# Kernel tuning notes

Hardware: AMD Instinct MI355X
Metric: run time of the kernel (lower is better)

## Reference

```python
import jax, jax.numpy as jnp
import numpy as np
import math

B, NTR, NTE = 4, 256, 64
S = NTR + NTE
FN, D = 64, 256
HF, HS = 8, 8
HC = HF // 2
HID = 4 * D


def _ln(x, g, b, eps=1e-5):
    m = jnp.mean(x, axis=-1, keepdims=True)
    v = jnp.mean((x - m) ** 2, axis=-1, keepdims=True)
    return (x - m) / jnp.sqrt(v + eps) * g + b


def _mha(q, k, v, Wq, bq, Wk, bk, Wv, bv, Wo, bo, H, mask):
    # PyTorch nn.MultiheadAttention (batch_first, eval): per-head scaled dot product
    Bq, Lq, Dm = q.shape
    Lk = k.shape[1]
    hd = Dm // H
    qh = (q @ Wq.T + bq).reshape(Bq, Lq, H, hd).transpose(0, 2, 1, 3)
    kh = (k @ Wk.T + bk).reshape(Bq, Lk, H, hd).transpose(0, 2, 1, 3)
    vh = (v @ Wv.T + bv).reshape(Bq, Lk, H, hd).transpose(0, 2, 1, 3)
    s = jnp.einsum('bhqd,bhkd->bhqk', qh, kh) / math.sqrt(hd)
    if mask is not None:
        s = s + mask  # broadcast (1,H,Lq,Lk)
    a = jax.nn.softmax(s, axis=-1)
    o = jnp.einsum('bhqk,bhkd->bhqd', a, vh).transpose(0, 2, 1, 3).reshape(Bq, Lq, Dm)
    return o @ Wo.T + bo


def setup_inputs() -> dict:
    key = jax.random.key(0)
    ks = jax.random.split(key, 64)
    i = [0]
    def w(shape, s=0.02):
        k = ks[i[0]]; i[0] += 1
        return jax.random.normal(k, shape, jnp.float32) * s
    inp = {}
    inp['x'] = jax.random.normal(ks[40], (B, S, FN, D), jnp.float32)
    m = jax.random.randint(ks[41], (FN, FN), 0, 2).astype(jnp.float32)
    inp['attn_mask'] = jnp.maximum(m, jnp.eye(FN, dtype=jnp.float32))  # keep diagonal unmasked
    for p in ['f', 't', 'e']:
        for n in ['Wq', 'Wk', 'Wv', 'Wo']:
            inp[n + p] = w((D, D))
        for n in ['bq', 'bk', 'bv', 'bo']:
            inp[n + p] = jnp.zeros((D,), jnp.float32)
        inp['g' + p] = jnp.ones((D,), jnp.float32)
        inp['b2' + p] = jnp.zeros((D,), jnp.float32)
    inp['W1'] = w((HID, D)); inp['b1'] = jnp.zeros((HID,), jnp.float32)
    inp['Wg'] = w((HID, D)); inp['bg'] = jnp.zeros((HID,), jnp.float32)
    inp['W2'] = w((D, HID)); inp['b2'] = jnp.zeros((D,), jnp.float32)
    inp['gm'] = jnp.ones((D,), jnp.float32); inp['bm'] = jnp.zeros((D,), jnp.float32)
    inp['N_train'] = NTR
    inp['N_test'] = NTE
    return inp


def reference(x, attn_mask, Wqf, Wkf, Wvf, Wof, bqf, bkf, bvf, bof, gf, b2f,
              Wqt, Wkt, Wvt, Wot, bqt, bkt, bvt, bot, gt, b2t,
              Wqe, Wke, Wve, Woe, bqe, bke, bve, boe, ge, b2e,
              W1, b1, Wg, bg, W2, b2, gm, bm, N_train, N_test):
    Bsz, Ssz, Fn, Dd = x.shape
    # --- feature attention with hybrid per-head mask ---
    x_row = x.reshape(Bsz * Ssz, Fn, Dd)
    xn = _ln(x_row, gf, b2f)
    additive = jnp.where(attn_mask == 1.0, 0.0, -jnp.inf).astype(x.dtype)  # (F,F)
    hybrid = jnp.concatenate([
        jnp.broadcast_to(additive[None], (HC, Fn, Fn)),
        jnp.zeros((HF - HC, Fn, Fn), x.dtype)], axis=0)[None]  # (1,H,F,F)
    x2 = _mha(xn, xn, xn, Wqf, bqf, Wkf, bkf, Wvf, bvf, Wof, bof, HF, hybrid)
    x_row = x_row + x2
    # --- sample attention (train self, test cross) ---
    x_col = x_row.reshape(Bsz, Ssz, Fn, Dd).transpose(0, 2, 1, 3).reshape(Bsz * Fn, Ssz, Dd)
    x_tr = x_col[:, :N_train]
    x_te = x_col[:, N_train:]
    tn = _ln(x_tr, gt, b2t)
    x_tr = x_tr + _mha(tn, tn, tn, Wqt, bqt, Wkt, bkt, Wvt, bvt, Wot, bot, HS, None)
    en = _ln(x_te, ge, b2e)
    kv = _ln(x_tr, ge, b2e)
    x_te = x_te + _mha(en, kv, kv, Wqe, bqe, Wke, bke, Wve, bve, Woe, boe, HS, None)
    x_col = jnp.concatenate([x_tr, x_te], axis=1)
    xo = x_col.reshape(Bsz, Fn, Ssz, Dd).transpose(0, 2, 1, 3)
    # --- SwiGLU MLP ---
    xn2 = _ln(xo, gm, bm)
    h = (xn2 @ W1.T + b1) * jax.nn.silu(xn2 @ Wg.T + bg)
    return xo + (h @ W2.T + b2)
```

## Files before the change

kernel.cpp:

```cpp
#include <hip/hip_runtime.h>
#include <hip/hip_bf16.h>

typedef __hip_bfloat16 bf16;
typedef __attribute__((ext_vector_type(8))) short short8v;
typedef __attribute__((ext_vector_type(4))) float f32x4;

#define Bz   4
#define Sz   320
#define FNz  64
#define Dz   256
#define HIDz 1024
#define TOK  (Bz*Sz*FNz)
#define NSEQ (Bz*FNz)
#define NTRz 256
#define NTEz 64
#define TTR  (NSEQ*NTRz)
#define TTE  (NSEQ*NTEz)
#define CHD  40960
#define SCALE 0.17677669529663687f

__device__ __forceinline__ size_t rowOff(int rr, int Ls, int s0){
  if (Ls == 0) return (size_t)rr * Dz;
  int n = rr / Ls;
  int s = rr - n * Ls + s0;
  return (((size_t)(n >> 6) * Sz + s) * FNz + (n & 63)) * Dz;
}

__device__ __forceinline__ void store4bf(bf16* p, float a, float b, float c, float d){
  bf16 t0=__float2bfloat16(a), t1=__float2bfloat16(b),
       t2=__float2bfloat16(c), t3=__float2bfloat16(d);
  ushort4 u;
  u.x=*(unsigned short*)&t0; u.y=*(unsigned short*)&t1;
  u.z=*(unsigned short*)&t2; u.w=*(unsigned short*)&t3;
  *(ushort4*)p = u;
}

__device__ __forceinline__ void store2bf(bf16* p, float a, float b){
  bf16 t0=__float2bfloat16(a), t1=__float2bfloat16(b);
  ushort2 u;
  u.x=*(unsigned short*)&t0; u.y=*(unsigned short*)&t1;
  *(ushort2*)p = u;
}

__device__ __forceinline__ void xcd_work(int ncols, int& row, int& col){
  int L   = blockIdx.x;
  int cpx = gridDim.x >> 3;
  int W   = (L & 7) * cpx + (L >> 3);
  row = W / ncols;
  col = W - row * ncols;
}

struct CvtArgs { const float* src[24]; bf16* dst[24]; };
__global__ __launch_bounds__(256) void cvt_multi(CvtArgs args){
  int i = (blockIdx.x * 256 + threadIdx.x) * 4;
  const float* s = args.src[blockIdx.y];
  bf16*        d = args.dst[blockIdx.y];
  float4 v = *(const float4*)(s + i);
  store4bf(d + i, v.x, v.y, v.z, v.w);
}

__global__ __launch_bounds__(256) void ln_kernel(const float* __restrict__ src,
    bf16* __restrict__ dst, const float* __restrict__ g, const float* __restrict__ b,
    int Ls, int s0){
  int rr   = blockIdx.x * 4 + (threadIdx.x >> 6);
  int lane = threadIdx.x & 63;
  size_t off = rowOff(rr, Ls, s0) + (size_t)lane * 4;
  float4 v = *(const float4*)(src + off);
  float s = v.x + v.y + v.z + v.w;
  float q = v.x*v.x + v.y*v.y + v.z*v.z + v.w*v.w;
  #pragma unroll
  for (int d = 1; d < 64; d <<= 1){ s += __shfl_xor(s, d); q += __shfl_xor(q, d); }
  float m   = s * (1.0f/Dz);
  float rsd = rsqrtf(q * (1.0f/Dz) - m*m + 1e-5f);
  float4 gv = *(const float4*)(g + lane*4);
  float4 bv = *(const float4*)(b + lane*4);
  store4bf(dst + (size_t)rr*Dz + lane*4,
           (v.x-m)*rsd*gv.x + bv.x, (v.y-m)*rsd*gv.y + bv.y,
           (v.z-m)*rsd*gv.z + bv.z, (v.w-m)*rsd*gv.w + bv.w);
}

template<int EPI>
__global__ __launch_bounds__(512) void mgemm(
    const bf16* __restrict__ A, const bf16* __restrict__ Wb,
    const float* __restrict__ bias, const float* __restrict__ biasB,
    const float* __restrict__ biasC, void* __restrict__ Cp,
    const float* __restrict__ resid, const bf16* __restrict__ aux,
    int M, int N, int K, int cLs, int cS0, int ncols){
  __shared__ __align__(16) char smemraw[30720];
  bf16 (*As)[40] = reinterpret_cast<bf16(*)[40]>(smemraw);
  bf16 (*Bs)[40] = reinterpret_cast<bf16(*)[40]>(smemraw + 10240);
  const int tid  = threadIdx.x;
  const int lane = tid & 63;
  const int wave = tid >> 6;
  int rowb, colb;
  xcd_work(ncols, rowb, colb);
  const int r0 = rowb * 128;
  const int n0 = colb * 256;
  const int srow = tid >> 2;
  const int scol = (tid & 3) * 8;
  const int bprow = (srow & 64) + (srow & 15)*4 + ((srow >> 4) & 3);
  const bf16* ap  = A  + (size_t)(r0 + srow) * K + scol;
  const bf16* bp0 = Wb + (size_t)(n0 + bprow) * K + scol;
  const bf16* bp1 = Wb + (size_t)(n0 + 128 + bprow) * K + scol;
  const int wr = wave >> 2, wc = wave & 3;
  const int fr = lane & 15;
  const int fk = (lane >> 4) * 8;
  f32x4 acc[4][4] = {};
  for (int k0 = 0; k0 < K; k0 += 32){
    uint4 av  = *(const uint4*)(ap  + k0);
    uint4 bv0 = *(const uint4*)(bp0 + k0);
    uint4 bv1 = *(const uint4*)(bp1 + k0);
    __syncthreads();
    *(uint4*)&As[srow][scol]       = av;
    *(uint4*)&Bs[srow][scol]       = bv0;
    *(uint4*)&Bs[128 + srow][scol] = bv1;
    __syncthreads();
    short8v af[4], bf[4];
    #pragma unroll
    for (int m = 0; m < 4; ++m)
      af[m] = *(const short8v*)&As[wr*64 + m*16 + fr][fk];
    #pragma unroll
    for (int n = 0; n < 4; ++n)
      bf[n] = *(const short8v*)&Bs[wc*64 + n*16 + fr][fk];
    #pragma unroll
    for (int m = 0; m < 4; ++m)
      #pragma unroll
      for (int n = 0; n < 4; ++n)
        acc[m][n] = __builtin_amdgcn_mfma_f32_16x16x32_bf16(af[m], bf[n], acc[m][n], 0, 0, 0);
  }
  const int er = (lane >> 4) * 4;
  if (EPI == 1){
    float* fsm = (float*)smemraw;
    const int cb = wc*64 + fr*4;
    float bb0 = bias[cb], bb1 = bias[cb+1], bb2 = bias[cb+2], bb3 = bias[cb+3];
    #pragma unroll
    for (int m = 0; m < 4; ++m){
      #pragma unroll
      for (int wrs = 0; wrs < 2; ++wrs){
        __syncthreads();
        if (wr == wrs){
          #pragma unroll
          for (int j = 0; j < 4; ++j){
            float4 t;
            t.x = acc[m][0][j] + bb0; t.y = acc[m][1][j] + bb1;
            t.z = acc[m][2][j] + bb2; t.w = acc[m][3][j] + bb3;
            *(float4*)&fsm[(er + j)*260 + cb] = t;
          }
        }
        __syncthreads();
        int rrow = r0 + wrs*64 + m*16 + (tid >> 5);
        size_t ro = rowOff(rrow, cLs, cS0) + (size_t)(tid & 31)*8;
        const float* fs = fsm + (tid >> 5)*260 + (tid & 31)*8;
        float4 v0 = *(const float4*)(fs);
        float4 v1 = *(const float4*)(fs + 4);
        float4 q0 = *(const float4*)(resid + ro);
        float4 q1 = *(const float4*)(resid + ro + 4);
        v0.x += q0.x; v0.y += q0.y; v0.z += q0.z; v0.w += q0.w;
        v1.x += q1.x; v1.y += q1.y; v1.z += q1.z; v1.w += q1.w;
        *(float4*)((float*)Cp + ro)     = v0;
        *(float4*)((float*)Cp + ro + 4) = v1;
      }
    }
  } else {
    const float* bp = bias;
    if (biasB != nullptr) bp = (colb == 0) ? bias : ((colb == 1) ? biasB : biasC);
    const int cl = wc*64 + fr*4;
    float bb0 = bp[cl], bb1 = bp[cl+1], bb2 = bp[cl+2], bb3 = bp[cl+3];
    const int cbase = n0 + cl;
    #pragma unroll
    for (int m = 0; m < 4; ++m){
      #pragma unroll
      for (int j = 0; j < 4; ++j){
        int r = r0 + wr*64 + m*16 + er + j;
        store4bf(&((bf16*)Cp)[(size_t)r * N + cbase],
                 acc[m][0][j] + bb0, acc[m][1][j] + bb1,
                 acc[m][2][j] + bb2, acc[m][3][j] + bb3);
      }
    }
  }
}

__global__ __launch_bounds__(512) void mgemm_dual(
    const bf16* __restrict__ A, const bf16* __restrict__ W1b,
    const bf16* __restrict__ Wgb, const float* __restrict__ b1,
    const float* __restrict__ bg, bf16* __restrict__ Hb,
    int M, int K){
  __shared__ bf16 As[128][40];
  __shared__ bf16 B1s[128][40];
  __shared__ bf16 B2s[128][40];
  const int tid  = threadIdx.x;
  const int lane = tid & 63;
  const int wave = tid >> 6;
  int rowb, colb;
  xcd_work(8, rowb, colb);
  const int r0 = rowb * 128;
  const int n0 = colb * 128;
  const int srow = tid >> 2;
  const int scol = (tid & 3) * 8;
  const int bprow = (srow & ~31) + (srow & 15)*2 + ((srow >> 4) & 1);
  const bf16* ap = A   + (size_t)(r0 + srow) * K + scol;
  const bf16* p1 = W1b + (size_t)(n0 + bprow) * K + scol;
  const bf16* p2 = Wgb + (size_t)(n0 + bprow) * K + scol;
  const int wr = wave >> 2, wc = wave & 3;
  const int fr = lane & 15;
  const int fk = (lane >> 4) * 8;
  f32x4 acc1[4][2] = {};
  f32x4 acc2[4][2] = {};
  for (int k0 = 0; k0 < K; k0 += 32){
    uint4 av = *(const uint4*)(ap + k0);
    uint4 v1 = *(const uint4*)(p1 + k0);
    uint4 v2 = *(const uint4*)(p2 + k0);
    __syncthreads();
    *(uint4*)&As[srow][scol]  = av;
    *(uint4*)&B1s[srow][scol] = v1;
    *(uint4*)&B2s[srow][scol] = v2;
    __syncthreads();
    short8v af[4], bf1[2], bf2[2];
    #pragma unroll
    for (int m = 0; m < 4; ++m)
      af[m] = *(const short8v*)&As[wr*64 + m*16 + fr][fk];
    #pragma unroll
    for (int n = 0; n < 2; ++n){
      bf1[n] = *(const short8v*)&B1s[wc*32 + n*16 + fr][fk];
      bf2[n] = *(const short8v*)&B2s[wc*32 + n*16 + fr][fk];
    }
    #pragma unroll
    for (int m = 0; m < 4; ++m)
      #pragma unroll
      for (int n = 0; n < 2; ++n){
        acc1[m][n] = __builtin_amdgcn_mfma_f32_16x16x32_bf16(af[m], bf1[n], acc1[m][n], 0, 0, 0);
        acc2[m][n] = __builtin_amdgcn_mfma_f32_16x16x32_bf16(af[m], bf2[n], acc2[m][n], 0, 0, 0);
      }
  }
  const int er = (lane >> 4) * 4;
  const int c = n0 + wc*32 + fr*2;
  const float b10 = b1[c], b11 = b1[c+1];
  const float bg0 = bg[c], bg1 = bg[c+1];
  #pragma unroll
  for (int m = 0; m < 4; ++m){
    #pragma unroll
    for (int j = 0; j < 4; ++j){
      int r = r0 + wr*64 + m*16 + er + j;
      float v0 = acc1[m][0][j] + b10;
      float g0 = acc2[m][0][j] + bg0;
      float v1 = acc1[m][1][j] + b11;
      float g1 = acc2[m][1][j] + bg1;
      float h0 = v0 * g0 / (1.0f + __expf(-g0));
      float h1 = v1 * g1 / (1.0f + __expf(-g1));
      store2bf(&Hb[(size_t)r * HIDz + c], h0, h1);
    }
  }
}

__global__ __launch_bounds__(256) void attn_t_m(
    const bf16* __restrict__ Q, const bf16* __restrict__ K,
    const bf16* __restrict__ V, bf16* __restrict__ O, int ld){
  __shared__ bf16 Klds[64][40];
  __shared__ bf16 Vt[32][72];
  __shared__ bf16 Plds[4][64][72];
  const int n = blockIdx.x, h = blockIdx.y;
  const int tid = threadIdx.x, lane = tid & 63, w = tid >> 6;
  const size_t ibase = (size_t)n * 256 * ld + (size_t)h * 32;
  const size_t obase = (size_t)n * 256 * Dz + (size_t)h * 32;
  const int l15 = lane & 15, l4 = lane >> 4;
  short8v qf[4];
  #pragma unroll
  for (int m = 0; m < 4; ++m)
    qf[m] = *(const short8v*)(Q + ibase + (size_t)(w*64 + m*16 + l15) * ld + l4*8);
  f32x4 accO[4][2] = {};
  float mrowq[4], lrowq[4], sclq[4];
  #pragma unroll
  for (int m=0;m<4;++m){ mrowq[m] = -1e30f; lrowq[m] = 0.f; }
  const f32x4 zero = {};
  for (int kb = 0; kb < 4; ++kb){
    __syncthreads();
    {
      int r = tid >> 2, c8 = (tid & 3) * 8;
      *(uint4*)&Klds[r][c8] = *(const uint4*)(K + ibase + (size_t)(kb*64 + r) * ld + c8);
      uint4 vr = *(const uint4*)(V + ibase + (size_t)(kb*64 + r) * ld + c8);
      const bf16* vb = (const bf16*)&vr;
      #pragma unroll
      for (int i = 0; i < 8; ++i) Vt[c8 + i][r] = vb[i];
    }
    __syncthreads();
    short8v kf[4];
    #pragma unroll
    for (int nn = 0; nn < 4; ++nn)
      kf[nn] = *(const short8v*)&Klds[nn*16 + l15][l4*8];
    f32x4 s2[4][4];
    #pragma unroll
    for (int m = 0; m < 4; ++m)
      #pragma unroll
      for (int nn = 0; nn < 4; ++nn)
        s2[m][nn] = __builtin_amdgcn_mfma_f32_16x16x32_bf16(kf[nn], qf[m], zero, 0,0,0);
    #pragma unroll
    for (int m = 0; m < 4; ++m){
      float mx = fmaxf(fmaxf(s2[m][0][0], s2[m][0][1]), fmaxf(s2[m][0][2], s2[m][0][3]));
      #pragma unroll
      for (int nn = 1; nn < 4; ++nn)
        mx = fmaxf(mx, fmaxf(fmaxf(s2[m][nn][0], s2[m][nn][1]),
                             fmaxf(s2[m][nn][2], s2[m][nn][3])));
      mx = fmaxf(mx, __shfl_xor(mx, 16));
      mx = fmaxf(mx, __shfl_xor(mx, 32));
      float mnew = fmaxf(mrowq[m], mx);
      float scl = __expf((mrowq[m] - mnew) * SCALE);
      mrowq[m] = mnew; sclq[m] = scl;
      float ps = 0.f;
      #pragma unroll
      for (int nn = 0; nn < 4; ++nn)
        #pragma unroll
        for (int j = 0; j < 4; ++j){
          float p = __expf((s2[m][nn][j] - mnew) * SCALE);
          s2[m][nn][j] = p; ps += p;
        }
      ps += __shfl_xor(ps, 16);
      ps += __shfl_xor(ps, 32);
      lrowq[m] = lrowq[m] * scl + ps;
    }
    #pragma unroll
    for (int m = 0; m < 4; ++m)
      #pragma unroll
      for (int j = 0; j < 4; ++j){
        float so = __shfl(sclq[m], l4*4 + j);
        accO[m][0][j] *= so; accO[m][1][j] *= so;
      }
    #pragma unroll
    for (int m = 0; m < 4; ++m)
      #pragma unroll
      for (int nn = 0; nn < 4; ++nn)
        store4bf(&Plds[w][m*16 + l15][nn*16 + l4*4],
                 s2[m][nn][0], s2[m][nn][1], s2[m][nn][2], s2[m][nn][3]);
    #pragma unroll
    for (int m = 0; m < 4; ++m){
      #pragma unroll
      for (int kt = 0; kt < 2; ++kt){
        short8v pf = *(const short8v*)&Plds[w][m*16 + l15][kt*32 + l4*8];
        #pragma unroll
        for (int dt = 0; dt < 2; ++dt){
          short8v vf = *(const short8v*)&Vt[dt*16 + l15][kt*32 + l4*8];
          accO[m][dt] = __builtin_amdgcn_mfma_f32_16x16x32_bf16(pf, vf, accO[m][dt], 0,0,0);
        }
      }
    }
  }
  #pragma unroll
  for (int m = 0; m < 4; ++m){
    #pragma unroll
    for (int j = 0; j < 4; ++j){
      float inv = 1.0f / __shfl(lrowq[m], l4*4 + j);
      int row = w*64 + m*16 + l4*4 + j;
      #pragma unroll
      for (int dt = 0; dt < 2; ++dt)
        O[obase + (size_t)row * Dz + dt*16 + l15] = __float2bfloat16(accO[m][dt][j] * inv);
    }
  }
}

template<int NKB, int MASK>
__global__ __launch_bounds__(256) void attn_w(
    const bf16* __restrict__ Q, const bf16* __restrict__ K,
    const bf16* __restrict__ V, const float* __restrict__ mask,
    bf16* __restrict__ O, int ldq, int ldkv){
  __shared__ bf16 Klds[4][64][40];
  __shared__ bf16 Vt[4][32][72];
  __shared__ bf16 Plds[4][64][72];
  const int r = blockIdx.x;
  const int tid = threadIdx.x, lane = tid & 63, w = tid >> 6;
  const int h = blockIdx.y * 4 + w;
  const int l15 = lane & 15, l4 = lane >> 4;
  const size_t qoff = (size_t)r * 64 * ldq + (size_t)h * 32;
  const size_t koff = (size_t)r * (NKB*64) * ldkv + (size_t)h * 32;
  const size_t ooff = (size_t)r * 64 * Dz + (size_t)h * 32;
  short8v qf[4];
  #pragma unroll
  for (int m = 0; m < 4; ++m)
    qf[m] = *(const short8v*)(Q + qoff + (size_t)(m*16 + l15) * ldq + l4*8);
  f32x4 accO[4][2] = {};
  float mrowq[4], lrowq[4], sclq[4];
  #pragma unroll
  for (int m=0;m<4;++m){ mrowq[m] = -1e30f; lrowq[m] = 0.f; }
  const f32x4 zero = {};
  for (int kb = 0; kb < NKB; ++kb){
    {
      const bf16* kp = K + koff + (size_t)(kb*64 + lane) * ldkv;
      const bf16* vp = V + koff + (size_t)(kb*64 + lane) * ldkv;
      uint4 k0 = *(const uint4*)(kp);      uint4 k1 = *(const uint4*)(kp + 8);
      uint4 k2 = *(const uint4*)(kp + 16); uint4 k3 = *(const uint4*)(kp + 24);
      *(uint4*)&Klds[w][lane][0]  = k0; *(uint4*)&Klds[w][lane][8]  = k1;
      *(uint4*)&Klds[w][lane][16] = k2; *(uint4*)&Klds[w][lane][24] = k3;
      uint4 v0 = *(const uint4*)(vp);      uint4 v1 = *(const uint4*)(vp + 8);
      uint4 v2 = *(const uint4*)(vp + 16); uint4 v3 = *(const uint4*)(vp + 24);
      const bf16* vb0=(const bf16*)&v0; const bf16* vb1=(const bf16*)&v1;
      const bf16* vb2=(const bf16*)&v2; const bf16* vb3=(const bf16*)&v3;
      #pragma unroll
      for (int i = 0; i < 8; ++i){
        Vt[w][i][lane]      = vb0[i];
        Vt[w][8 + i][lane]  = vb1[i];
        Vt[w][16 + i][lane] = vb2[i];
        Vt[w][24 + i][lane] = vb3[i];
      }
    }
    short8v kf[4];
    #pragma unroll
    for (int nn = 0; nn < 4; ++nn)
      kf[nn] = *(const short8v*)&Klds[w][nn*16 + l15][l4*8];
    f32x4 s2[4][4];
    #pragma unroll
    for (int m = 0; m < 4; ++m)
      #pragma unroll
      for (int nn = 0; nn < 4; ++nn)
        s2[m][nn] = __builtin_amdgcn_mfma_f32_16x16x32_bf16(kf[nn], qf[m], zero, 0,0,0);
    if (MASK && h < 4){
      #pragma unroll
      for (int m = 0; m < 4; ++m)
        #pragma unroll
        for (int nn = 0; nn < 4; ++nn)
          #pragma unroll
          for (int j = 0; j < 4; ++j){
            int qq = m*16 + l15, kk = nn*16 + l4*4 + j;
            s2[m][nn][j] += (mask[qq*64 + kk] == 1.0f ? 0.0f : -1e30f);
          }
    }
    #pragma unroll
    for (int m = 0; m < 4; ++m){
      float mx = fmaxf(fmaxf(s2[m][0][0], s2[m][0][1]), fmaxf(s2[m][0][2], s2[m][0][3]));
      #pragma unroll
      for (int nn = 1; nn < 4; ++nn)
        mx = fmaxf(mx, fmaxf(fmaxf(s2[m][nn][0], s2[m][nn][1]),
                             fmaxf(s2[m][nn][2], s2[m][nn][3])));
      mx = fmaxf(mx, __shfl_xor(mx, 16));
      mx = fmaxf(mx, __shfl_xor(mx, 32));
      float mnew = fmaxf(mrowq[m], mx);
      float scl = __expf((mrowq[m] - mnew) * SCALE);
      mrowq[m] = mnew; sclq[m] = scl;
      float ps = 0.f;
      #pragma unroll
      for (int nn = 0; nn < 4; ++nn)
        #pragma unroll
        for (int j = 0; j < 4; ++j){
          float p = __expf((s2[m][nn][j] - mnew) * SCALE);
          s2[m][nn][j] = p; ps += p;
        }
      ps += __shfl_xor(ps, 16);
      ps += __shfl_xor(ps, 32);
      lrowq[m] = lrowq[m] * scl + ps;
    }
    #pragma unroll
    for (int m = 0; m < 4; ++m)
      #pragma unroll
      for (int j = 0; j < 4; ++j){
        float so = __shfl(sclq[m], l4*4 + j);
        accO[m][0][j] *= so; accO[m][1][j] *= so;
      }
    #pragma unroll
    for (int m = 0; m < 4; ++m)
      #pragma unroll
      for (int nn = 0; nn < 4; ++nn)
        store4bf(&Plds[w][m*16 + l15][nn*16 + l4*4],
                 s2[m][nn][0], s2[m][nn][1], s2[m][nn][2], s2[m][nn][3]);
    #pragma unroll
    for (int m = 0; m < 4; ++m){
      #pragma unroll
      for (int kt = 0; kt < 2; ++kt){
        short8v pf = *(const short8v*)&Plds[w][m*16 + l15][kt*32 + l4*8];
        #pragma unroll
        for (int dt = 0; dt < 2; ++dt){
          short8v vf = *(const short8v*)&Vt[w][dt*16 + l15][kt*32 + l4*8];
          accO[m][dt] = __builtin_amdgcn_mfma_f32_16x16x32_bf16(pf, vf, accO[m][dt], 0,0,0);
        }
      }
    }
  }
  #pragma unroll
  for (int m = 0; m < 4; ++m){
    #pragma unroll
    for (int j = 0; j < 4; ++j){
      float inv = 1.0f / __shfl(lrowq[m], l4*4 + j);
      int row = m*16 + l4*4 + j;
      #pragma unroll
      for (int dt = 0; dt < 2; ++dt)
        O[ooff + (size_t)row * Dz + dt*16 + l15] = __float2bfloat16(accO[m][dt][j] * inv);
    }
  }
}

extern "C" void kernel_launch(void* const* d_in, const int* in_sizes, int n_in,
                              void* d_out, int out_size, void* d_ws, size_t ws_size,
                              hipStream_t stream){
  (void)in_sizes; (void)n_in; (void)out_size; (void)ws_size;
  const float* x    = (const float*)d_in[0];
  const float* mask = (const float*)d_in[1];
  const float *Wqf=(const float*)d_in[2],  *Wkf=(const float*)d_in[3],
              *Wvf=(const float*)d_in[4],  *Wof=(const float*)d_in[5],
              *bqf=(const float*)d_in[6],  *bkf=(const float*)d_in[7],
              *bvf=(const float*)d_in[8],  *bof=(const float*)d_in[9],
              *gf =(const float*)d_in[10], *b2f=(const float*)d_in[11];
  const float *Wqt=(const float*)d_in[12], *Wkt=(const float*)d_in[13],
              *Wvt=(const float*)d_in[14], *Wot=(const float*)d_in[15],
              *bqt=(const float*)d_in[16], *bkt=(const float*)d_in[17],
              *bvt=(const float*)d_in[18], *bot=(const float*)d_in[19],
              *gt =(const float*)d_in[20], *b2t=(const float*)d_in[21];
  const float *Wqe=(const float*)d_in[22], *Wke=(const float*)d_in[23],
              *Wve=(const float*)d_in[24], *Woe=(const float*)d_in[25],
              *bqe=(const float*)d_in[26], *bke=(const float*)d_in[27],
              *bve=(const float*)d_in[28], *boe=(const float*)d_in[29],
              *ge =(const float*)d_in[30], *b2e=(const float*)d_in[31];
  const float *W1=(const float*)d_in[32], *b1=(const float*)d_in[33],
              *Wg=(const float*)d_in[34], *bg=(const float*)d_in[35],
              *W2=(const float*)d_in[36], *b2v=(const float*)d_in[37],
              *gm=(const float*)d_in[38], *bm=(const float*)d_in[39];

  float* Y = (float*)d_out;

  char* wsb = (char*)d_ws;
  size_t off = 0;
  auto carve = [&](size_t bytes)->void*{
    void* p = wsb + off; off += (bytes + 255) & ~(size_t)255; return p;
  };
  bf16* Xn   = (bf16*)carve((size_t)TOK * Dz * 2);
  bf16* QKVb = (bf16*)carve((size_t)TOK * 768 * 2);
  bf16* Ob   = (bf16*)carve((size_t)TOK * Dz * 2);
  bf16* Hb   = (bf16*)carve((size_t)CHD * HIDz * 2);
  bf16* WQKVf = (bf16*)carve((size_t)768*256*2);
  bf16* WQKVt = (bf16*)carve((size_t)768*256*2);
  bf16* WKVe  = (bf16*)carve((size_t)512*256*2);
  bf16* Wqeb  = (bf16*)carve((size_t)256*256*2);
  bf16* Wofb  = (bf16*)carve((size_t)256*256*2);
  bf16* Wotb  = (bf16*)carve((size_t)256*256*2);
  bf16* Woeb  = (bf16*)carve((size_t)256*256*2);
  bf16* W1b   = (bf16*)carve((size_t)HIDz*256*2);
  bf16* Wgb   = (bf16*)carve((size_t)HIDz*256*2);
  bf16* W2b   = (bf16*)carve((size_t)256*HIDz*2);

  const int DD = Dz*Dz;
  {
    CvtArgs ca;
    const float* s12[12] = {Wqf,Wkf,Wvf, Wqt,Wkt,Wvt, Wke,Wve, Wqe,Wof,Wot,Woe};
    bf16* d12[12] = {WQKVf,WQKVf+DD,WQKVf+2*DD, WQKVt,WQKVt+DD,WQKVt+2*DD,
                     WKVe,WKVe+DD, Wqeb,Wofb,Wotb,Woeb};
    for (int i = 0; i < 12; ++i){ ca.src[i] = s12[i]; ca.dst[i] = d12[i]; }
    const float* sh[3] = {W1, Wg, W2};
    bf16* dh[3] = {W1b, Wgb, W2b};
    for (int j = 0; j < 3; ++j)
      for (int p = 0; p < 4; ++p){
        ca.src[12 + j*4 + p] = sh[j] + (size_t)p * DD;
        ca.dst[12 + j*4 + p] = dh[j] + (size_t)p * DD;
      }
    cvt_multi<<<dim3(DD/1024, 24), 256, 0, stream>>>(ca);
  }

  bf16* Qeb = QKVb + (size_t)TTR * 512;

  ln_kernel<<<TOK/4, 256, 0, stream>>>(x, Xn, gf, b2f, 0, 0);
  mgemm<0><<<3*(TOK/128), 512, 0, stream>>>(Xn, WQKVf, bqf, bkf, bvf, QKVb,
      nullptr, nullptr, TOK, 768, 256, 0,0, 3);
  attn_w<1,1><<<dim3(Bz*Sz, 2), 256, 0, stream>>>(QKVb, QKVb+256, QKVb+512, mask, Ob, 768, 768);
  mgemm<1><<<TOK/128, 512, 0, stream>>>(Ob, Wofb, bof, nullptr, nullptr, Y,
      x, nullptr, TOK, 256, 256, 0,0, 1);

  ln_kernel<<<TTR/4, 256, 0, stream>>>(Y, Xn, gt, b2t, NTRz, 0);
  mgemm<0><<<3*(TTR/128), 512, 0, stream>>>(Xn, WQKVt, bqt, bkt, bvt, QKVb,
      nullptr, nullptr, TTR, 768, 256, 0,0, 3);
  attn_t_m<<<dim3(NSEQ, 8), 256, 0, stream>>>(QKVb, QKVb+256, QKVb+512, Ob, 768);
  mgemm<1><<<TTR/128, 512, 0, stream>>>(Ob, Wotb, bot, nullptr, nullptr, Y,
      Y, nullptr, TTR, 256, 256, NTRz,0, 1);

  ln_kernel<<<TTR/4, 256, 0, stream>>>(Y, Xn, ge, b2e, NTRz, 0);
  ln_kernel<<<TTE/4, 256, 0, stream>>>(Y, Xn + (size_t)TTR*Dz, ge, b2e, NTEz, NTRz);
  mgemm<0><<<TTE/128, 512, 0, stream>>>(Xn + (size_t)TTR*Dz, Wqeb, bqe,
      nullptr, nullptr, Qeb, nullptr, nullptr, TTE, 256, 256, 0,0, 1);
  mgemm<0><<<2*(TTR/128), 512, 0, stream>>>(Xn, WKVe, bke, bve, bve, QKVb,
      nullptr, nullptr, TTR, 512, 256, 0,0, 2);
  attn_w<4,0><<<dim3(NSEQ, 2), 256, 0, stream>>>(Qeb, QKVb, QKVb+256, nullptr, Ob, 256, 512);
  mgemm<1><<<TTE/128, 512, 0, stream>>>(Ob, Woeb, boe, nullptr, nullptr, Y,
      Y, nullptr, TTE, 256, 256, NTEz,NTRz, 1);

  ln_kernel<<<TOK/4, 256, 0, stream>>>(Y, Xn, gm, bm, 0, 0);
  for (int c = 0; c < TOK/CHD; ++c){
    const bf16* Anc = Xn + (size_t)c * CHD * Dz;
    float*      Yc  = Y  + (size_t)c * CHD * Dz;
    mgemm_dual<<<8*(CHD/128), 512, 0, stream>>>(Anc, W1b, Wgb, b1, bg,
        Hb, CHD, 256);
    mgemm<1><<<CHD/128, 512, 0, stream>>>(Hb, W2b, b2v, nullptr, nullptr,
        Yc, Yc, nullptr, CHD, 256, HIDz, 0,0, 1);
  }
}
```

Measured before the change: 719.9 us.

## Fuse downstream LayerNorms into residual-add GEMM epilogues

```diff
diff --git a/kernel.cpp b/kernel.cpp
--- a/kernel.cpp
+++ b/kernel.cpp
@@ -50,6 +50,28 @@
   col = W - row * ncols;
 }
 
+__device__ __forceinline__ void halfwave_ln(float4 v0, float4 v1,
+                                            float& mean, float& rsd){
+  float s = v0.x+v0.y+v0.z+v0.w + v1.x+v1.y+v1.z+v1.w;
+  float q = v0.x*v0.x+v0.y*v0.y+v0.z*v0.z+v0.w*v0.w
+          + v1.x*v1.x+v1.y*v1.y+v1.z*v1.z+v1.w*v1.w;
+  #pragma unroll
+  for (int d = 1; d < 32; d <<= 1){ s += __shfl_xor(s, d); q += __shfl_xor(q, d); }
+  mean = s * (1.0f/Dz);
+  rsd  = rsqrtf(q * (1.0f/Dz) - mean*mean + 1e-5f);
+}
+
+__device__ __forceinline__ void ln_emit(bf16* dp, int c0, float4 v0, float4 v1,
+                                        float mean, float rsd,
+                                        const float* G, const float* B){
+  float4 g0 = *(const float4*)(G + c0), g1 = *(const float4*)(G + c0 + 4);
+  float4 b0 = *(const float4*)(B + c0), b1 = *(const float4*)(B + c0 + 4);
+  store4bf(dp + c0,     (v0.x-mean)*rsd*g0.x + b0.x, (v0.y-mean)*rsd*g0.y + b0.y,
+                        (v0.z-mean)*rsd*g0.z + b0.z, (v0.w-mean)*rsd*g0.w + b0.w);
+  store4bf(dp + c0 + 4, (v1.x-mean)*rsd*g1.x + b1.x, (v1.y-mean)*rsd*g1.y + b1.y,
+                        (v1.z-mean)*rsd*g1.z + b1.z, (v1.w-mean)*rsd*g1.w + b1.w);
+}
+
 struct CvtArgs { const float* src[24]; bf16* dst[24]; };
 __global__ __launch_bounds__(256) void cvt_multi(CvtArgs args){
   int i = (blockIdx.x * 256 + threadIdx.x) * 4;
@@ -79,13 +101,15 @@
            (v.z-m)*rsd*gv.z + bv.z, (v.w-m)*rsd*gv.w + bv.w);
 }
 
-template<int EPI>
+template<int EPI, int FUSE>
 __global__ __launch_bounds__(512) void mgemm(
     const bf16* __restrict__ A, const bf16* __restrict__ Wb,
     const float* __restrict__ bias, const float* __restrict__ biasB,
     const float* __restrict__ biasC, void* __restrict__ Cp,
     const float* __restrict__ resid, const bf16* __restrict__ aux,
-    int M, int N, int K, int cLs, int cS0, int ncols){
+    int M, int N, int K, int cLs, int cS0, int ncols,
+    const float* lnGa, const float* lnBa, const float* lnGb, const float* lnBb,
+    bf16* dstA, bf16* dstB){
   __shared__ __align__(16) char smemraw[30720];
   bf16 (*As)[40] = reinterpret_cast<bf16(*)[40]>(smemraw);
   bf16 (*Bs)[40] = reinterpret_cast<bf16(*)[40]>(smemraw + 10240);
@@ -149,8 +173,9 @@
         }
         __syncthreads();
         int rrow = r0 + wrs*64 + m*16 + (tid >> 5);
-        size_t ro = rowOff(rrow, cLs, cS0) + (size_t)(tid & 31)*8;
-        const float* fs = fsm + (tid >> 5)*260 + (tid & 31)*8;
+        int c0 = (tid & 31) * 8;
+        size_t ro = rowOff(rrow, cLs, cS0) + c0;
+        const float* fs = fsm + (tid >> 5)*260 + c0;
         float4 v0 = *(const float4*)(fs);
         float4 v1 = *(const float4*)(fs + 4);
         float4 q0 = *(const float4*)(resid + ro);
@@ -159,6 +184,29 @@
         v1.x += q1.x; v1.y += q1.y; v1.z += q1.z; v1.w += q1.w;
         *(float4*)((float*)Cp + ro)     = v0;
         *(float4*)((float*)Cp + ro + 4) = v1;
+        if (FUSE > 0){
+          float mean, rsd;
+          halfwave_ln(v0, v1, mean, rsd);
+          if (FUSE == 1){
+            int b = rrow / (Sz*FNz);
+            int rem = rrow - b*(Sz*FNz);
+            int s = rem >> 6, f = rem & 63;
+            int n = (b << 6) + f;
+            if (s < NTRz)
+              ln_emit(dstA + (size_t)(n*NTRz + s)*Dz, c0, v0, v1, mean, rsd, lnGa, lnBa);
+            else
+              ln_emit(dstB + (size_t)(n*NTEz + s - NTRz)*Dz, c0, v0, v1, mean, rsd, lnGb, lnBb);
+          } else if (FUSE == 2){
+            int n = rrow >> 8, s = rrow & 255;
+            int b = n >> 6, f = n & 63;
+            ln_emit(dstA + (size_t)rrow*Dz, c0, v0, v1, mean, rsd, lnGa, lnBa);
+            ln_emit(dstB + (size_t)((b*Sz + s)*FNz + f)*Dz, c0, v0, v1, mean, rsd, lnGb, lnBb);
+          } else {
+            int n = rrow >> 6, t = rrow & 63;
+            int b = n >> 6, f = n & 63, s = t + NTRz;
+            ln_emit(dstB + (size_t)((b*Sz + s)*FNz + f)*Dz, c0, v0, v1, mean, rsd, lnGb, lnBb);
+          }
+        }
       }
     }
   } else {
@@ -532,6 +580,10 @@
   bf16* Wgb   = (bf16*)carve((size_t)HIDz*256*2);
   bf16* W2b   = (bf16*)carve((size_t)256*HIDz*2);
 
+  bf16* XnD = QKVb + (size_t)TOK * 512;
+  bf16* Xnq = Xn + (size_t)TTR * Dz;
+  bf16* Qeb = QKVb + (size_t)TTR * 512;
+
   const int DD = Dz*Dz;
   {
     CvtArgs ca;
@@ -549,39 +601,42 @@
     cvt_multi<<<dim3(DD/1024, 24), 256, 0, stream>>>(ca);
   }
 
-  bf16* Qeb = QKVb + (size_t)TTR * 512;
-
   ln_kernel<<<TOK/4, 256, 0, stream>>>(x, Xn, gf, b2f, 0, 0);
-  mgemm<0><<<3*(TOK/128), 512, 0, stream>>>(Xn, WQKVf, bqf, bkf, bvf, QKVb,
-      nullptr, nullptr, TOK, 768, 256, 0,0, 3);
+  mgemm<0,0><<<3*(TOK/128), 512, 0, stream>>>(Xn, WQKVf, bqf, bkf, bvf, QKVb,
+      nullptr, nullptr, TOK, 768, 256, 0,0, 3,
+      nullptr,nullptr,nullptr,nullptr, nullptr,nullptr);
   attn_w<1,1><<<dim3(Bz*Sz, 2), 256, 0, stream>>>(QKVb, QKVb+256, QKVb+512, mask, Ob, 768, 768);
-  mgemm<1><<<TOK/128, 512, 0, stream>>>(Ob, Wofb, bof, nullptr, nullptr, Y,
-      x, nullptr, TOK, 256, 256, 0,0, 1);
-
-  ln_kernel<<<TTR/4, 256, 0, stream>>>(Y, Xn, gt, b2t, NTRz, 0);
-  mgemm<0><<<3*(TTR/128), 512, 0, stream>>>(Xn, WQKVt, bqt, bkt, bvt, QKVb,
-      nullptr, nullptr, TTR, 768, 256, 0,0, 3);
+  mgemm<1,1><<<TOK/128, 512, 0, stream>>>(Ob, Wofb, bof, nullptr, nullptr, Y,
+      x, nullptr, TOK, 256, 256, 0,0, 1,
+      gt, b2t, ge, b2e, Xn, Xnq);
+
+  mgemm<0,0><<<3*(TTR/128), 512, 0, stream>>>(Xn, WQKVt, bqt, bkt, bvt, QKVb,
+      nullptr, nullptr, TTR, 768, 256, 0,0, 3,
+      nullptr,nullptr,nullptr,nullptr, nullptr,nullptr);
   attn_t_m<<<dim3(NSEQ, 8), 256, 0, stream>>>(QKVb, QKVb+256, QKVb+512, Ob, 768);
-  mgemm<1><<<TTR/128, 512, 0, stream>>>(Ob, Wotb, bot, nullptr, nullptr, Y,
-      Y, nullptr, TTR, 256, 256, NTRz,0, 1);
-
-  ln_kernel<<<TTR/4, 256, 0, stream>>>(Y, Xn, ge, b2e, NTRz, 0);
-  ln_kernel<<<TTE/4, 256, 0, stream>>>(Y, Xn + (size_t)TTR*Dz, ge, b2e, NTEz, NTRz);
-  mgemm<0><<<TTE/128, 512, 0, stream>>>(Xn + (size_t)TTR*Dz, Wqeb, bqe,
-      nullptr, nullptr, Qeb, nullptr, nullptr, TTE, 256, 256, 0,0, 1);
-  mgemm<0><<<2*(TTR/128), 512, 0, stream>>>(Xn, WKVe, bke, bve, bve, QKVb,
-      nullptr, nullptr, TTR, 512, 256, 0,0, 2);
-  attn_w<4,0><<<dim3(NSEQ, 2), 256, 0, stream>>>(Qeb, QKVb, QKVb+256, nullptr, Ob, 256, 512);
-  mgemm<1><<<TTE/128, 512, 0, stream>>>(Ob, Woeb, boe, nullptr, nullptr, Y,
-      Y, nullptr, TTE, 256, 256, NTEz,NTRz, 1);
-
-  ln_kernel<<<TOK/4, 256, 0, stream>>>(Y, Xn, gm, bm, 0, 0);
+  mgemm<1,2><<<TTR/128, 512, 0, stream>>>(Ob, Wotb, bot, nullptr, nullptr, Y,
+      Y, nullptr, TTR, 256, 256, NTRz,0, 1,
+      ge, b2e, gm, bm, Xn, XnD);
+
+  mgemm<0,0><<<TTE/128, 512, 0, stream>>>(Xnq, Wqeb, bqe,
+      nullptr, nullptr, Qeb, nullptr, nullptr, TTE, 256, 256, 0,0, 1,
+      nullptr,nullptr,nullptr,nullptr, nullptr,nullptr);
+  mgemm<0,0><<<2*(TTR/128), 512, 0, stream>>>(Xn, WKVe, bke, bve, bve, QKVb,
+      nullptr, nullptr, TTR, 512, 256, 0,0, 2,
+      nullptr,nullptr,nullptr,nullptr, nullptr,nullptr);
+  attn_w<4,0><<<dim3(NSEQ, 2), 256, 0, stream>>>(Qeb, QKVb, QKVb+256,
+      nullptr, Ob, 256, 512);
+  mgemm<1,3><<<TTE/128, 512, 0, stream>>>(Ob, Woeb, boe, nullptr, nullptr, Y,
+      Y, nullptr, TTE, 256, 256, NTEz,NTRz, 1,
+      nullptr, nullptr, gm, bm, nullptr, XnD);
+
   for (int c = 0; c < TOK/CHD; ++c){
-    const bf16* Anc = Xn + (size_t)c * CHD * Dz;
-    float*      Yc  = Y  + (size_t)c * CHD * Dz;
+    const bf16* Anc = XnD + (size_t)c * CHD * Dz;
+    float*      Yc  = Y   + (size_t)c * CHD * Dz;
     mgemm_dual<<<8*(CHD/128), 512, 0, stream>>>(Anc, W1b, Wgb, b1, bg,
         Hb, CHD, 256);
-    mgemm<1><<<CHD/128, 512, 0, stream>>>(Hb, W2b, b2v, nullptr, nullptr,
-        Yc, Yc, nullptr, CHD, 256, HIDz, 0,0, 1);
-  }
-}
+    mgemm<1,0><<<CHD/128, 512, 0, stream>>>(Hb, W2b, b2v, nullptr, nullptr,
+        Yc, Yc, nullptr, CHD, 256, HIDz, 0,0, 1,
+        nullptr,nullptr,nullptr,nullptr, nullptr,nullptr);
+  }
+}
```

Measured after the change: 750.5 us. +4.3%, slower.
